# Kernel optimization log

Hardware: AMD Instinct MI355X
Metric: run time of the kernel (lower is better)

## Reference

```python
import jax, jax.numpy as jnp
import numpy as np

B, N, E, H = 1, 4096, 2048, 16
D = E // H  # head_size = 128
DEGREE = 4
LN_EPS = 1e-5
ROPE_BASE = 10000.0


def rope_cos_sin(n, d):
    # [n, d//2] tables
    inv_freq = 1.0 / (ROPE_BASE ** (jnp.arange(0, d, 2, dtype=jnp.float32) / d))
    t = jnp.arange(n, dtype=jnp.float32)[:, None] * inv_freq[None, :]
    return jnp.cos(t), jnp.sin(t)


def apply_rope(x, cos, sin):
    # x: [b, n, h, d]; rotate-half RoPE
    x1, x2 = jnp.split(x, 2, axis=-1)
    c = cos[None, :, None, :]
    s = sin[None, :, None, :]
    return jnp.concatenate([x1 * c - x2 * s, x1 * s + x2 * c], axis=-1)


def layernorm(x, scale, bias, eps=LN_EPS):
    m = jnp.mean(x, axis=-1, keepdims=True)
    v = jnp.var(x, axis=-1, keepdims=True)
    return (x - m) * jax.lax.rsqrt(v + eps) * scale + bias


def polynomial_attention(q, k, v, degree, is_causal):
    # q,k,v: [b, h, n, d]
    a = jnp.einsum('bhnd,bhmd->bhnm', q, k) ** degree
    if is_causal:
        a = jnp.tril(a)
    denom = jnp.sum(a, axis=-1, keepdims=True)
    return jnp.einsum('bhnm,bhmd->bhnd', a / denom, v)


def setup_inputs() -> dict:
    key = jax.random.key(0)
    k0, k1, k2 = jax.random.split(key, 3)
    x = jax.random.normal(k0, (B, N, E), dtype=jnp.float32)
    # Dense(3*emb_dim, use_bias=False) and Dense(emb_dim, use_bias=False)
    w_qkv = jax.random.normal(k1, (E, 3 * E), dtype=jnp.float32) * (1.0 / np.sqrt(E))
    w_out = jax.random.normal(k2, (E, E), dtype=jnp.float32) * (1.0 / np.sqrt(E))
    # shared pre-attention LayerNorm over head dim (flax init: scale=1, bias=0)
    ln_scale = jnp.ones((D,), dtype=jnp.float32)
    ln_bias = jnp.zeros((D,), dtype=jnp.float32)
    return {"x": x, "w_qkv": w_qkv, "w_out": w_out,
            "ln_scale": ln_scale, "ln_bias": ln_bias}


def reference(x, w_qkv, w_out, ln_scale, ln_bias):
    b, n, e = x.shape
    proj = x @ w_qkv                              # [b, n, 3e]
    q, k, v = jnp.split(proj, 3, axis=-1)
    q = q.reshape(b, n, H, D)
    k = k.reshape(b, n, H, D)
    v = v.reshape(b, n, H, D)
    cos, sin = rope_cos_sin(n, D)
    q = apply_rope(q, cos, sin)
    k = apply_rope(k, cos, sin)
    # transpose branch (non-softmax): [b, h, n, d]
    q = q.transpose(0, 2, 1, 3)
    k = k.transpose(0, 2, 1, 3)
    v = v.transpose(0, 2, 1, 3)
    # shared pre_attn LayerNorm applied to q and k
    q = layernorm(q, ln_scale, ln_bias)
    k = layernorm(k, ln_scale, ln_bias)
    out = polynomial_attention(q, k, v, DEGREE, True)  # [b, h, n, d]
    out = out.transpose(0, 2, 1, 3).reshape(b, n, e)
    out = out @ w_out                              # dropout rate 0 / inference: identity
    return out
```

## Files before the change

kernel.cpp:

```cpp
#include <hip/hip_runtime.h>
#include <stdint.h>
#include <math.h>

#define N_SEQ 4096
#define EDIM  2048
#define NH    16
#define HD    128

typedef __attribute__((ext_vector_type(8))) short bf16x8;
typedef __attribute__((ext_vector_type(4))) float f32x4;

#define AS1 __attribute__((address_space(1)))
#define AS3 __attribute__((address_space(3)))

__device__ __forceinline__ void gll16(const unsigned short* g, unsigned short* l) {
    __builtin_amdgcn_global_load_lds((const AS1 unsigned int*)g,
                                     (AS3 unsigned int*)l, 16, 0, 0);
}

__device__ __forceinline__ unsigned short f2bf(float f) {
    union { float f; unsigned u; } v; v.f = f;
    unsigned r = v.u + 0x7FFFu + ((v.u >> 16) & 1u);
    return (unsigned short)(r >> 16);
}
__device__ __forceinline__ float bf2f(unsigned short h) {
    union { unsigned u; float f; } v; v.u = ((unsigned)h) << 16;
    return v.f;
}

__global__ void k_convert_x(const float* __restrict__ x,
                            unsigned short* __restrict__ xb, int n4) {
    int i = blockIdx.x * blockDim.x + threadIdx.x;
    int stride = gridDim.x * blockDim.x;
    for (; i < n4; i += stride) {
        float4 v = ((const float4*)x)[i];
        ushort4 o;
        o.x = f2bf(v.x); o.y = f2bf(v.y); o.z = f2bf(v.z); o.w = f2bf(v.w);
        ((ushort4*)xb)[i] = o;
    }
}

__global__ void k_transpose_f32_bf16(const float* __restrict__ in,
                                     unsigned short* __restrict__ out,
                                     int R, int C) {
    __shared__ unsigned short Ls[64][68];
    const int c0 = blockIdx.x * 64, r0 = blockIdx.y * 64;
    const int t = threadIdx.x;
    #pragma unroll
    for (int i = 0; i < 4; ++i) {
        int ch = i * 256 + t;
        int r = ch >> 4, c4 = (ch & 15) * 4;
        float4 v = *(const float4*)&in[(size_t)(r0 + r) * C + c0 + c4];
        ushort4 o;
        o.x = f2bf(v.x); o.y = f2bf(v.y); o.z = f2bf(v.z); o.w = f2bf(v.w);
        *(ushort4*)&Ls[r][c4] = o;
    }
    __syncthreads();
    #pragma unroll
    for (int i = 0; i < 2; ++i) {
        int ch = i * 256 + t;
        int rr = ch >> 3, c8 = (ch & 7) * 8;
        unsigned short vals[8];
        #pragma unroll
        for (int j = 0; j < 8; ++j) vals[j] = Ls[c8 + j][rr];
        uint4 pk;
        pk.x = (unsigned)vals[0] | ((unsigned)vals[1] << 16);
        pk.y = (unsigned)vals[2] | ((unsigned)vals[3] << 16);
        pk.z = (unsigned)vals[4] | ((unsigned)vals[5] << 16);
        pk.w = (unsigned)vals[6] | ((unsigned)vals[7] << 16);
        *(uint4*)&out[(size_t)(c0 + rr) * R + r0 + c8] = pk;
    }
}

template<int F32OUT>
__launch_bounds__(256, 2)
__global__ void k_gemm_bt(const unsigned short* __restrict__ A,
                          const unsigned short* __restrict__ Bt,
                          void* __restrict__ C,
                          int M, int N, int K) {
    __shared__ unsigned short sh[2 * 128 * 64];
    unsigned short* As = sh;
    unsigned short* Bs = sh + 128 * 64;

    const int t = threadIdx.x;
    const int wave = t >> 6, lane = t & 63;
    const int wm = wave >> 1, wn = wave & 1;
    const int lg = lane >> 4, lr = lane & 15;

    const int nbx = gridDim.x;
    const int nwg = nbx * gridDim.y;
    int bid = blockIdx.y * nbx + blockIdx.x;
    int swz = (bid & 7) * (nwg >> 3) + (bid >> 3);
    const int m0 = (swz / nbx) * 128;
    const int n0 = (swz % nbx) * 128;

    const unsigned short* aptr = A  + (size_t)m0 * K;
    const unsigned short* bptr = Bt + (size_t)n0 * K;

    f32x4 acc[4][4];
    #pragma unroll
    for (int i = 0; i < 4; ++i)
        #pragma unroll
        for (int j = 0; j < 4; ++j) acc[i][j] = f32x4{0.f, 0.f, 0.f, 0.f};

    int schr[4], srow[4], scb[4];
    #pragma unroll
    for (int i = 0; i < 4; ++i) {
        int ch = (i * 4 + wave) * 64 + lane;
        schr[i] = ch;
        srow[i] = ch >> 3;
        scb[i]  = (ch & 7) ^ ((ch >> 3) & 7);
    }

    const int nkb = K >> 6;
    for (int kb = 0; kb < nkb; ++kb) {
        __syncthreads();
        #pragma unroll
        for (int i = 0; i < 4; ++i) {
            const size_t goff = (size_t)srow[i] * K + (size_t)kb * 64 + scb[i] * 8;
            gll16(&aptr[goff], &As[schr[i] * 8]);
            gll16(&bptr[goff], &Bs[schr[i] * 8]);
        }
        __syncthreads();

        #pragma unroll
        for (int kk = 0; kk < 2; ++kk) {
            bf16x8 af[4], bf[4];
            const int cbx = ((kk * 4 + lg) ^ (lr & 7)) * 8;
            #pragma unroll
            for (int i = 0; i < 4; ++i) {
                af[i] = *(const bf16x8*)&As[(wm * 64 + i * 16 + lr) * 64 + cbx];
                bf[i] = *(const bf16x8*)&Bs[(wn * 64 + i * 16 + lr) * 64 + cbx];
            }
            #pragma unroll
            for (int i = 0; i < 4; ++i)
                #pragma unroll
                for (int j = 0; j < 4; ++j)
                    acc[i][j] = __builtin_amdgcn_mfma_f32_16x16x32_bf16(af[i], bf[j], acc[i][j], 0, 0, 0);
        }
    }

    if (F32OUT) {
        #pragma unroll
        for (int i = 0; i < 4; ++i) {
            int row0 = m0 + wm * 64 + i * 16 + lg * 4;
            #pragma unroll
            for (int j = 0; j < 4; ++j) {
                int col = n0 + wn * 64 + j * 16 + lr;
                #pragma unroll
                for (int r = 0; r < 4; ++r)
                    ((float*)C)[(size_t)(row0 + r) * N + col] = acc[i][j][r];
            }
        }
    } else {
        __syncthreads();
        unsigned short* Cs = sh;
        #pragma unroll
        for (int i = 0; i < 4; ++i) {
            #pragma unroll
            for (int j = 0; j < 4; ++j) {
                int col = wn * 64 + j * 16 + lr;
                #pragma unroll
                for (int r = 0; r < 4; ++r)
                    Cs[(wm * 64 + i * 16 + lg * 4 + r) * 128 + col] = f2bf(acc[i][j][r]);
            }
        }
        __syncthreads();
        #pragma unroll
        for (int i = 0; i < 8; ++i) {
            int ch = i * 256 + t;
            int row = ch >> 4, c8 = (ch & 15) * 8;
            *(uint4*)&((unsigned short*)C)[(size_t)(m0 + row) * N + n0 + c8] =
                *(const uint4*)&Cs[row * 128 + c8];
        }
    }
}

__global__ void k_ropeln(const unsigned short* __restrict__ proj,
                         const float* __restrict__ ln_scale,
                         const float* __restrict__ ln_bias,
                         unsigned short* __restrict__ Qh,
                         unsigned short* __restrict__ Kh) {
    const int n = blockIdx.x;
    const int wave = threadIdx.x >> 6, lane = threadIdx.x & 63;
    float inv = expf(-((float)(2 * lane) / 128.0f) * 9.210340371976184f);
    float ang = (float)n * inv;
    float c = cosf(ang), s = sinf(ang);
    const float sc1 = ln_scale[lane], sc2 = ln_scale[lane + 64];
    const float b1 = ln_bias[lane],  b2 = ln_bias[lane + 64];

    for (int r = wave; r < 32; r += 4) {
        int h = r >> 1, qk = r & 1;
        const unsigned short* src = proj + (size_t)n * (3 * EDIM) + qk * EDIM + h * HD;
        float x1 = bf2f(src[lane]), x2 = bf2f(src[lane + 64]);
        float o1 = x1 * c - x2 * s;
        float o2 = x1 * s + x2 * c;
        float sum = o1 + o2, sq = o1 * o1 + o2 * o2;
        #pragma unroll
        for (int d = 1; d < 64; d <<= 1) {
            sum += __shfl_xor(sum, d);
            sq  += __shfl_xor(sq, d);
        }
        float mean = sum * (1.0f / 128.0f);
        float var = sq * (1.0f / 128.0f) - mean * mean;
        float rstd = rsqrtf(var + 1e-5f);
        float y1 = (o1 - mean) * rstd * sc1 + b1;
        float y2 = (o2 - mean) * rstd * sc2 + b2;
        unsigned short* dst = (qk ? Kh : Qh) + ((size_t)h * N_SEQ + n) * HD;
        dst[lane]      = f2bf(y1);
        dst[lane + 64] = f2bf(y2);
    }
}

__global__ void k_vtrans(const unsigned short* __restrict__ proj,
                         unsigned short* __restrict__ Vt) {
    __shared__ unsigned short Ls[64][136];
    const int h = blockIdx.y;
    const int n0 = blockIdx.x * 64;
    const int t = threadIdx.x;
    #pragma unroll
    for (int i = 0; i < 4; ++i) {
        int ch = i * 256 + t;
        int r = ch >> 4, d0 = (ch & 15) * 8;
        uint4 v = *(const uint4*)&proj[(size_t)(n0 + r) * (3 * EDIM) + 2 * EDIM + h * HD + d0];
        *(uint4*)&Ls[r][d0] = v;
    }
    __syncthreads();
    #pragma unroll
    for (int i = 0; i < 4; ++i) {
        int ch = i * 256 + t;
        int d = ch >> 3, nb = (ch & 7) * 8;
        unsigned short vals[8];
        #pragma unroll
        for (int j = 0; j < 8; ++j) vals[j] = Ls[nb + j][d];
        uint4 pk;
        pk.x = (unsigned)vals[0] | ((unsigned)vals[1] << 16);
        pk.y = (unsigned)vals[2] | ((unsigned)vals[3] << 16);
        pk.z = (unsigned)vals[4] | ((unsigned)vals[5] << 16);
        pk.w = (unsigned)vals[6] | ((unsigned)vals[7] << 16);
        *(uint4*)&Vt[((size_t)h * HD + d) * N_SEQ + n0 + nb] = pk;
    }
}

__launch_bounds__(256, 2)
__global__ void k_attn(const unsigned short* __restrict__ Qh,
                       const unsigned short* __restrict__ Kh,
                       const unsigned short* __restrict__ Vt,
                       unsigned short* __restrict__ O) {
    __shared__ unsigned short pool[4 * 8192];

    const int t = threadIdx.x;
    const int w = t >> 6, lane = t & 63;
    const int lg = lane >> 4, lr = lane & 15;

    const int s = blockIdx.x & 255;
    const int batch = blockIdx.x >> 8;
    const int x = s & 7;
    const int hb = (s >> 3) & 1;
    const int h = x * 2 + hb;
    const int qq = s >> 4;
    const int qb = batch ? qq : (31 - qq);
    const int q0 = qb * 128;
    const int qbase = q0 + w * 32;

    bf16x8 qf[2][4];
    #pragma unroll
    for (int mi = 0; mi < 2; ++mi)
        #pragma unroll
        for (int kk = 0; kk < 4; ++kk)
            qf[mi][kk] = *(const bf16x8*)&Qh[((size_t)h * N_SEQ + qbase + mi * 16 + lr) * HD + kk * 32 + lg * 8];

    f32x4 acc[2][8];
    #pragma unroll
    for (int i = 0; i < 2; ++i)
        #pragma unroll
        for (int j = 0; j < 8; ++j) acc[i][j] = f32x4{0.f, 0.f, 0.f, 0.f};
    f32x4 accd[2];
    accd[0] = f32x4{0.f, 0.f, 0.f, 0.f};
    accd[1] = f32x4{0.f, 0.f, 0.f, 0.f};

    bf16x8 onesf;
    {
        short ov = (lr == 0) ? (short)0x3F80 : (short)0;
        #pragma unroll
        for (int j = 0; j < 8; ++j) onesf[j] = ov;
    }

    int kch[4], vch[4];
    const unsigned short* kg[4];
    const unsigned short* vg[4];
    #pragma unroll
    for (int i = 0; i < 4; ++i) {
        int ch = i * 256 + t;
        kch[i] = ch;
        int r = ch >> 4, p = ch & 15;
        int csrc = (p & 8) | ((p ^ r) & 7);
        kg[i] = Kh + ((size_t)h * N_SEQ + r) * HD + csrc * 8;
    }
    #pragma unroll
    for (int i = 0; i < 4; ++i) {
        int ch = i * 256 + t;
        vch[i] = ch;
        int d = ch >> 3, p2 = ch & 7;
        int c2src = (p2 ^ d) & 7;
        vg[i] = Vt + ((size_t)h * HD + d) * N_SEQ + c2src * 8;
    }

    const int nkb = 2 * qb + 2;

    {
        #pragma unroll
        for (int i = 0; i < 4; ++i) { gll16(kg[i], pool + kch[i] * 8); kg[i] += 64 * HD; }
        #pragma unroll
        for (int i = 0; i < 4; ++i) { gll16(vg[i], pool + 16384 + vch[i] * 8); vg[i] += 64; }
    }

    union U8 { unsigned u[4]; bf16x8 v; };

    for (int kb = 0; kb < nkb; ++kb) {
        const int cur = kb & 1;
        const int k0 = kb * 64;

        if (kb + 1 < nkb) {
            const int nxt = cur ^ 1;
            unsigned short* Kn = pool + nxt * 8192;
            unsigned short* Vn = pool + 16384 + nxt * 8192;
            #pragma unroll
            for (int i = 0; i < 4; ++i) { gll16(kg[i], Kn + kch[i] * 8); kg[i] += 64 * HD; }
            #pragma unroll
            for (int i = 0; i < 4; ++i) { gll16(vg[i], Vn + vch[i] * 8); vg[i] += 64; }
            asm volatile("s_waitcnt vmcnt(8)" ::: "memory");
        } else {
            asm volatile("s_waitcnt vmcnt(0)" ::: "memory");
        }
        __builtin_amdgcn_s_barrier();

        const unsigned short* Kc = pool + cur * 8192;
        const unsigned short* Vc = pool + 16384 + cur * 8192;

        f32x4 sa[2][4];
        #pragma unroll
        for (int i = 0; i < 2; ++i)
            #pragma unroll
            for (int j = 0; j < 4; ++j) sa[i][j] = f32x4{0.f, 0.f, 0.f, 0.f};
        #pragma unroll
        for (int nn = 0; nn < 2; ++nn) {
            bf16x8 kf[2][4];
            #pragma unroll
            for (int nj = 0; nj < 2; ++nj)
                #pragma unroll
                for (int kk = 0; kk < 4; ++kk) {
                    int row = (nn * 2 + nj) * 16 + lr;
                    int c = kk * 4 + lg;
                    int cs = (c & 8) | ((c ^ row) & 7);
                    kf[nj][kk] = *(const bf16x8*)&Kc[row * 128 + cs * 8];
                }
            __builtin_amdgcn_s_setprio(1);
            #pragma unroll
            for (int kk = 0; kk < 4; ++kk)
                #pragma unroll
                for (int nj = 0; nj < 2; ++nj)
                    #pragma unroll
                    for (int mi = 0; mi < 2; ++mi)
                        sa[mi][nn * 2 + nj] = __builtin_amdgcn_mfma_f32_16x16x32_bf16(
                            kf[nj][kk], qf[mi][kk], sa[mi][nn * 2 + nj], 0, 0, 0);
            __builtin_amdgcn_s_setprio(0);
        }

        unsigned wreg[2][4][2];
        const bool nomask = (k0 + 63 <= qbase);
        #pragma unroll
        for (int mi = 0; mi < 2; ++mi)
            #pragma unroll
            for (int nj = 0; nj < 4; ++nj) {
                float p[4];
                #pragma unroll
                for (int r = 0; r < 4; ++r) {
                    float sv = sa[mi][nj][r];
                    float t2 = sv * sv;
                    p[r] = t2 * t2;
                    if (!nomask) {
                        int gk = k0 + nj * 16 + lg * 4 + r;
                        int gq = qbase + mi * 16 + lr;
                        p[r] = (gk <= gq) ? p[r] : 0.0f;
                    }
                }
                asm("v_cvt_pk_bf16_f32 %0, %1, %2" : "=v"(wreg[mi][nj][0]) : "v"(p[0]), "v"(p[1]));
                asm("v_cvt_pk_bf16_f32 %0, %1, %2" : "=v"(wreg[mi][nj][1]) : "v"(p[2]), "v"(p[3]));
            }

        #pragma unroll
        for (int s2 = 0; s2 < 2; ++s2) {
            bf16x8 pa[2];
            #pragma unroll
            for (int mi = 0; mi < 2; ++mi) {
                U8 u;
                u.u[0] = wreg[mi][2 * s2][0];
                u.u[1] = wreg[mi][2 * s2][1];
                u.u[2] = wreg[mi][2 * s2 + 1][0];
                u.u[3] = wreg[mi][2 * s2 + 1][1];
                pa[mi] = u.v;
            }
            __builtin_amdgcn_s_setprio(1);
            #pragma unroll
            for (int ni = 0; ni < 8; ++ni) {
                int d = ni * 16 + lr;
                int base = d * 64 + (lg & 1) * 4;
                int cA = ((s2 * 4 + (lg >> 1)) ^ d) & 7;
                int cB = ((s2 * 4 + 2 + (lg >> 1)) ^ d) & 7;
                uint2 va = *(const uint2*)&Vc[base + cA * 8];
                uint2 vb = *(const uint2*)&Vc[base + cB * 8];
                U8 tv;
                tv.u[0] = va.x; tv.u[1] = va.y; tv.u[2] = vb.x; tv.u[3] = vb.y;
                #pragma unroll
                for (int mi = 0; mi < 2; ++mi)
                    acc[mi][ni] = __builtin_amdgcn_mfma_f32_16x16x32_bf16(pa[mi], tv.v, acc[mi][ni], 0, 0, 0);
            }
            #pragma unroll
            for (int mi = 0; mi < 2; ++mi)
                accd[mi] = __builtin_amdgcn_mfma_f32_16x16x32_bf16(pa[mi], onesf, accd[mi], 0, 0, 0);
            __builtin_amdgcn_s_setprio(0);
        }

        __builtin_amdgcn_s_barrier();
    }

    unsigned short* Cs = pool;
    #pragma unroll
    for (int mi = 0; mi < 2; ++mi) {
        #pragma unroll
        for (int r = 0; r < 4; ++r) {
            float dv = __shfl(accd[mi][r], lane & 48);
            float rinv = 1.0f / dv;
            int rw = w * 32 + mi * 16 + lg * 4 + r;
            #pragma unroll
            for (int ni = 0; ni < 8; ++ni)
                Cs[rw * 128 + ni * 16 + lr] = f2bf(acc[mi][ni][r] * rinv);
        }
    }
    __syncthreads();
    #pragma unroll
    for (int i = 0; i < 8; ++i) {
        int ch = i * 256 + t;
        int row = ch >> 4, c8 = (ch & 15) * 8;
        *(uint4*)&O[(size_t)(q0 + row) * EDIM + h * HD + c8] = *(const uint4*)&Cs[row * 128 + c8];
    }
}

extern "C" void kernel_launch(void* const* d_in, const int* in_sizes, int n_in,
                              void* d_out, int out_size, void* d_ws, size_t ws_size,
                              hipStream_t stream) {
    const float* x        = (const float*)d_in[0];
    const float* w_qkv    = (const float*)d_in[1];
    const float* w_out    = (const float*)d_in[2];
    const float* ln_scale = (const float*)d_in[3];
    const float* ln_bias  = (const float*)d_in[4];

    if (ws_size < 134217728u) return;

    char* ws = (char*)d_ws;
    unsigned short* xb    = (unsigned short*)(ws);
    unsigned short* wqkvT = (unsigned short*)(ws + 16777216);
    unsigned short* woutT = (unsigned short*)(ws + 41943040);
    unsigned short* proj  = (unsigned short*)(ws + 50331648);
    unsigned short* Kh    = (unsigned short*)(ws + 100663296);
    unsigned short* Vt    = (unsigned short*)(ws + 117440512);
    unsigned short* Qh    = wqkvT;
    unsigned short* attnO = xb;

    k_convert_x<<<2048, 256, 0, stream>>>(x, xb, (N_SEQ * EDIM) / 4);
    k_transpose_f32_bf16<<<dim3(3 * EDIM / 64, EDIM / 64), 256, 0, stream>>>(w_qkv, wqkvT, EDIM, 3 * EDIM);
    k_transpose_f32_bf16<<<dim3(EDIM / 64, EDIM / 64), 256, 0, stream>>>(w_out, woutT, EDIM, EDIM);
    k_gemm_bt<0><<<dim3(3 * EDIM / 128, N_SEQ / 128), 256, 0, stream>>>(xb, wqkvT, proj, N_SEQ, 3 * EDIM, EDIM);
    k_ropeln<<<N_SEQ, 256, 0, stream>>>(proj, ln_scale, ln_bias, Qh, Kh);
    k_vtrans<<<dim3(N_SEQ / 64, NH), 256, 0, stream>>>(proj, Vt);
    k_attn<<<512, 256, 0, stream>>>(Qh, Kh, Vt, attnO);
    k_gemm_bt<1><<<dim3(EDIM / 128, N_SEQ / 128), 256, 0, stream>>>(attnO, woutT, (float*)d_out, N_SEQ, EDIM, EDIM);
}
```

Baseline: 312.8 us.

## Permute V transpose layout for single 16-byte LDS reads and unroll double-buffer loop

The V-transpose kernel now writes each 8-element chunk with a permuted key order, so the attention kernel can fetch a full bf16x8 V fragment with one 16-byte LDS read instead of two 8-byte reads plus a register shuffle. The main K/V loop is also manually unrolled by two, with fixed buffer pointers for each half, which removes the runtime buffer-index arithmetic. This relies on nkb always being even and on the permutation matching the MFMA operand layout used for P.

After: 305.4 us. 2.4% less time.

```diff
diff --git a/kernel.cpp b/kernel.cpp
--- a/kernel.cpp
+++ b/kernel.cpp
@@ -229,16 +229,19 @@
     #pragma unroll
     for (int i = 0; i < 4; ++i) {
         int ch = i * 256 + t;
-        int d = ch >> 3, nb = (ch & 7) * 8;
+        int d = ch >> 3, p = ch & 7;
         unsigned short vals[8];
         #pragma unroll
-        for (int j = 0; j < 8; ++j) vals[j] = Ls[nb + j][d];
+        for (int j = 0; j < 8; ++j) {
+            int ko = 32 * (p >> 2) + 16 * (j >> 2) + 4 * (p & 3) + (j & 3);
+            vals[j] = Ls[ko][d];
+        }
         uint4 pk;
         pk.x = (unsigned)vals[0] | ((unsigned)vals[1] << 16);
         pk.y = (unsigned)vals[2] | ((unsigned)vals[3] << 16);
         pk.z = (unsigned)vals[4] | ((unsigned)vals[5] << 16);
         pk.w = (unsigned)vals[6] | ((unsigned)vals[7] << 16);
-        *(uint4*)&Vt[((size_t)h * HD + d) * N_SEQ + n0 + nb] = pk;
+        *(uint4*)&Vt[((size_t)h * HD + d) * N_SEQ + n0 + p * 8] = pk;
     }
 }
 
@@ -308,36 +311,16 @@
 
     const int nkb = 2 * qb + 2;
 
-    {
-        #pragma unroll
-        for (int i = 0; i < 4; ++i) { gll16(kg[i], pool + kch[i] * 8); kg[i] += 64 * HD; }
-        #pragma unroll
-        for (int i = 0; i < 4; ++i) { gll16(vg[i], pool + 16384 + vch[i] * 8); vg[i] += 64; }
-    }
-
     union U8 { unsigned u[4]; bf16x8 v; };
 
-    for (int kb = 0; kb < nkb; ++kb) {
-        const int cur = kb & 1;
-        const int k0 = kb * 64;
-
-        if (kb + 1 < nkb) {
-            const int nxt = cur ^ 1;
-            unsigned short* Kn = pool + nxt * 8192;
-            unsigned short* Vn = pool + 16384 + nxt * 8192;
-            #pragma unroll
-            for (int i = 0; i < 4; ++i) { gll16(kg[i], Kn + kch[i] * 8); kg[i] += 64 * HD; }
-            #pragma unroll
-            for (int i = 0; i < 4; ++i) { gll16(vg[i], Vn + vch[i] * 8); vg[i] += 64; }
-            asm volatile("s_waitcnt vmcnt(8)" ::: "memory");
-        } else {
-            asm volatile("s_waitcnt vmcnt(0)" ::: "memory");
-        }
-        __builtin_amdgcn_s_barrier();
-
-        const unsigned short* Kc = pool + cur * 8192;
-        const unsigned short* Vc = pool + 16384 + cur * 8192;
-
+    auto stage = [&](unsigned short* Kn, unsigned short* Vn) {
+        #pragma unroll
+        for (int i = 0; i < 4; ++i) { gll16(kg[i], Kn + kch[i] * 8); kg[i] += 64 * HD; }
+        #pragma unroll
+        for (int i = 0; i < 4; ++i) { gll16(vg[i], Vn + vch[i] * 8); vg[i] += 64; }
+    };
+
+    auto compute = [&](int k0, const unsigned short* Kc, const unsigned short* Vc) {
         f32x4 sa[2][4];
         #pragma unroll
         for (int i = 0; i < 2; ++i)
@@ -405,23 +388,35 @@
             #pragma unroll
             for (int ni = 0; ni < 8; ++ni) {
                 int d = ni * 16 + lr;
-                int base = d * 64 + (lg & 1) * 4;
-                int cA = ((s2 * 4 + (lg >> 1)) ^ d) & 7;
-                int cB = ((s2 * 4 + 2 + (lg >> 1)) ^ d) & 7;
-                uint2 va = *(const uint2*)&Vc[base + cA * 8];
-                uint2 vb = *(const uint2*)&Vc[base + cB * 8];
-                U8 tv;
-                tv.u[0] = va.x; tv.u[1] = va.y; tv.u[2] = vb.x; tv.u[3] = vb.y;
+                int cs = ((s2 * 4 + lg) ^ (d & 7)) & 7;
+                bf16x8 vf = *(const bf16x8*)&Vc[d * 64 + cs * 8];
                 #pragma unroll
                 for (int mi = 0; mi < 2; ++mi)
-                    acc[mi][ni] = __builtin_amdgcn_mfma_f32_16x16x32_bf16(pa[mi], tv.v, acc[mi][ni], 0, 0, 0);
+                    acc[mi][ni] = __builtin_amdgcn_mfma_f32_16x16x32_bf16(pa[mi], vf, acc[mi][ni], 0, 0, 0);
             }
             #pragma unroll
             for (int mi = 0; mi < 2; ++mi)
                 accd[mi] = __builtin_amdgcn_mfma_f32_16x16x32_bf16(pa[mi], onesf, accd[mi], 0, 0, 0);
             __builtin_amdgcn_s_setprio(0);
         }
-
+    };
+
+    stage(pool, pool + 16384);
+
+    for (int kb = 0; kb < nkb; kb += 2) {
+        stage(pool + 8192, pool + 16384 + 8192);
+        asm volatile("s_waitcnt vmcnt(8)" ::: "memory");
+        __builtin_amdgcn_s_barrier();
+        compute(kb * 64, pool, pool + 16384);
+        __builtin_amdgcn_s_barrier();
+        if (kb + 2 < nkb) {
+            stage(pool, pool + 16384);
+            asm volatile("s_waitcnt vmcnt(8)" ::: "memory");
+        } else {
+            asm volatile("s_waitcnt vmcnt(0)" ::: "memory");
+        }
+        __builtin_amdgcn_s_barrier();
+        compute((kb + 1) * 64, pool + 8192, pool + 16384 + 8192);
         __builtin_amdgcn_s_barrier();
     }
 
```
